# Performance work log

Hardware: AMD Instinct MI355X
Metric: run time of the kernel (lower is better)

The kernel has to match this reference:

```python
import jax, jax.numpy as jnp
import numpy as np

# ---- static config (mirrors CE defaults) ----
PS = 7        # patch size
WS = 27       # search window (per side)
S0 = 4        # query stride (stride0)
KS = 100      # k_s: top-k kept by search
KA = 100      # k_a: top-k used for aggregation
SCALE = 10.0  # softmax_scale
CI = 16       # inter_channels


def conv2d(x, w, b, pad):
    y = jax.lax.conv_general_dilated(
        x, w, (1, 1), [(pad, pad), (pad, pad)],
        dimension_numbers=("NCHW", "OIHW", "NCHW"))
    return y + b[None, :, None, None]


def all_patches(v):
    """[T,C,H,W] -> [T, H*W, C*PS*PS]; top-left anchored PSxPS patches,
    edge-clamped at the border (dnls-style bounded patch extraction)."""
    t, c, h, w = v.shape
    ii = jnp.clip(jnp.arange(h)[:, None] + jnp.arange(PS)[None, :], 0, h - 1)
    jj = jnp.clip(jnp.arange(w)[:, None] + jnp.arange(PS)[None, :], 0, w - 1)
    p = v[:, :, ii][:, :, :, :, jj]          # [T,C,H,PS,W,PS]
    p = p.transpose(0, 2, 4, 1, 3, 5)        # [T,H,W,C,PS,PS]
    return p.reshape(t, h * w, c * PS * PS)


def setup_inputs():
    key = jax.random.key(0)
    ks = jax.random.split(key, 4)
    vid = jax.random.normal(ks[0], (4, 64, 128, 128), jnp.float32)
    g_w = jax.random.normal(ks[1], (CI, 64, 3, 3), jnp.float32) * 0.05
    g_b = jnp.zeros((CI,), jnp.float32)
    theta_w = jax.random.normal(ks[2], (CI, 64, 1, 1), jnp.float32) * 0.1
    theta_b = jnp.zeros((CI,), jnp.float32)
    return {"vid": vid, "g_w": g_w, "g_b": g_b,
            "theta_w": theta_w, "theta_b": theta_b}


def reference(vid, g_w, g_b, theta_w, theta_b):
    t, c, h, w = vid.shape
    nH, nW = h // S0, w // S0
    Q, N = nH * nW, h * w

    # feature extraction (g -> search features, theta -> aggregation values)
    v1 = conv2d(vid, g_w, g_b, 1)          # [T,CI,H,W]
    v2 = conv2d(vid, theta_w, theta_b, 0)  # [T,CI,H,W]

    # windowed k-NN patch search: query grid (stride0) vs all keys (stride1=1)
    P1 = all_patches(v1)                                    # [T,N,D]
    qis = jnp.arange(nH) * S0
    qjs = jnp.arange(nW) * S0
    qflat = (qis[:, None] * w + qjs[None, :]).reshape(-1)   # [Q]
    Pq = P1[:, qflat]                                       # [T,Q,D]
    scores = jnp.einsum("tqd,tnd->tqn", Pq, P1)             # [T,Q,N]

    off = jnp.arange(WS) - WS // 2
    ci = jnp.clip(qis[:, None] + off, 0, h - 1)             # [nH,WS]
    cj = jnp.clip(qjs[:, None] + off, 0, w - 1)             # [nW,WS]
    cand = (ci[:, None, :, None] * w + cj[None, :, None, :]).reshape(Q, WS * WS)
    dists = jnp.take_along_axis(scores, cand[None], axis=2)  # [T,Q,WS*WS]

    d_k, widx = jax.lax.top_k(dists, KS)                    # [T,Q,KS]
    inds = jnp.take_along_axis(jnp.broadcast_to(cand[None], dists.shape),
                               widx, axis=2)                # flat key positions

    # top-k softmax aggregation weights
    wgt = jax.nn.softmax(d_k[..., :KA] * SCALE, axis=-1)    # [T,Q,KA]
    inds_a = inds[..., :KA]

    # wpsum: weighted sum of value patches gathered at neighbor indices,
    # expressed as sparse-scatter matrix @ dense patch matrix
    A = jnp.zeros((t, Q, N), scores.dtype).at[
        jnp.arange(t)[:, None, None],
        jnp.arange(Q)[None, :, None],
        inds_a].add(wgt)                                    # [T,Q,N]
    P2 = all_patches(v2)                                    # [T,N,D]
    z = jnp.einsum("tqn,tnd->tqd", A, P2)                   # [T,Q,CI*PS*PS]

    # ifold: scatter-add overlapping patches + count normalization
    z = z.reshape(t, Q, CI, PS, PS).transpose(0, 2, 1, 3, 4)
    z = z.reshape(t, CI, Q * PS * PS)
    ri = jnp.clip(qis[:, None] + jnp.arange(PS), 0, h - 1)  # [nH,PS]
    rj = jnp.clip(qjs[:, None] + jnp.arange(PS), 0, w - 1)  # [nW,PS]
    pix = (ri[:, None, :, None] * w + rj[None, :, None, :]).reshape(-1)
    Y = jnp.zeros((t, CI, N), z.dtype).at[:, :, pix].add(z)
    Zc = jnp.zeros((N,), z.dtype).at[pix].add(1.0)
    y = (Y / Zc).reshape(t, CI, h, w)
    return y
```

## Files before the change

### kernel.cpp

```cpp
#include <hip/hip_runtime.h>
#include <hip/hip_bf16.h>

#define T_ 4
#define C_ 64
#define H_ 128
#define W_ 128
#define CI_ 16
#define PS_ 7
#define NC_ 729
#define S0_ 4
#define KS_ 100
#define NQ_ 1024
#define SCALE_ 10.0f
#define HW_ (H_*W_)
#define RW_ 45
#define LCAP_ 768
#define CB_ 8

typedef float v2f __attribute__((ext_vector_type(2)));
#if __has_builtin(__builtin_elementwise_fma)
#define VFMA(a, b, c) __builtin_elementwise_fma((a), (b), (c))
#else
#define VFMA(a, b, c) ((a) * (b) + (c))
#endif

__device__ __forceinline__ float4 colfix(float4 r, bool loB, bool hiB) {
  float4 o;
  o.x = loB ? 0.f : (hiB ? r.y : r.x);
  o.y = loB ? r.x : (hiB ? r.z : r.y);
  o.z = loB ? r.y : (hiB ? r.w : r.z);
  o.w = loB ? r.z : (hiB ? 0.f : r.w);
  return o;
}

__global__ __launch_bounds__(128, 1) void conv3x3_kernel(
    const float* __restrict__ vid, const float* __restrict__ gw,
    const float* __restrict__ gb, float4* __restrict__ v1cs) {
  __shared__ float wls[C_ * 9 * 4];
  const int tid = threadIdx.x;
  const int g = blockIdx.y, t = blockIdx.z;
  for (int m = tid; m < C_ * 9 * 4; m += 128) {
    int co = m & 3, ck = m >> 2;
    wls[m] = gw[((size_t)(g * 4 + co) * C_) * 9 + ck];
  }
  __syncthreads();
  const int ti0 = (blockIdx.x >> 3) * 16, tj0 = (blockIdx.x & 7) * 16;
  const int u = tid >> 3, v = tid & 7;
  const int i = ti0 + u, j0 = tj0 + 2 * v;
  const int c0 = j0 - 1;
  const int c0c = min(max(c0, 0), W_ - 4);
  const bool loB = (c0 < 0), hiB = (c0 > W_ - 4);
  const int rm1 = max(i - 1, 0), rp1 = min(i + 1, H_ - 1);
  const float mk0 = (i > 0) ? 1.f : 0.f;
  const float mk2 = (i < H_ - 1) ? 1.f : 0.f;
  const int o0 = rm1 * W_ + c0c, o1 = i * W_ + c0c, o2 = rp1 * W_ + c0c;

  float accA[4], accB[4];
#pragma unroll
  for (int co = 0; co < 4; ++co) { accA[co] = gb[g * 4 + co]; accB[co] = gb[g * 4 + co]; }

  const float* vb = vid + ((size_t)t * C_) * HW_;
#pragma unroll 1
  for (int cb = 0; cb < C_; cb += CB_) {
    float4 r[CB_][3];
#pragma unroll
    for (int c = 0; c < CB_; ++c) {
      const float* p = vb + (size_t)(cb + c) * HW_;
      r[c][0] = *(const float4*)(p + o0);
      r[c][1] = *(const float4*)(p + o1);
      r[c][2] = *(const float4*)(p + o2);
    }
#pragma unroll
    for (int c = 0; c < CB_; ++c) {
      float4 f0 = colfix(r[c][0], loB, hiB);
      float4 f1 = colfix(r[c][1], loB, hiB);
      float4 f2 = colfix(r[c][2], loB, hiB);
      f0.x *= mk0; f0.y *= mk0; f0.z *= mk0; f0.w *= mk0;
      f2.x *= mk2; f2.y *= mk2; f2.z *= mk2; f2.w *= mk2;
      const float* wc = &wls[(cb + c) * 36];
      float e0[4] = {f0.x, f0.y, f0.z, f0.w};
      float e1[4] = {f1.x, f1.y, f1.z, f1.w};
      float e2[4] = {f2.x, f2.y, f2.z, f2.w};
#pragma unroll
      for (int kj = 0; kj < 3; ++kj) {
#pragma unroll
        for (int co = 0; co < 4; ++co) {
          accA[co] = fmaf(wc[(0 * 3 + kj) * 4 + co], e0[kj],     accA[co]);
          accB[co] = fmaf(wc[(0 * 3 + kj) * 4 + co], e0[kj + 1], accB[co]);
          accA[co] = fmaf(wc[(1 * 3 + kj) * 4 + co], e1[kj],     accA[co]);
          accB[co] = fmaf(wc[(1 * 3 + kj) * 4 + co], e1[kj + 1], accB[co]);
          accA[co] = fmaf(wc[(2 * 3 + kj) * 4 + co], e2[kj],     accA[co]);
          accB[co] = fmaf(wc[(2 * 3 + kj) * 4 + co], e2[kj + 1], accB[co]);
        }
      }
    }
  }
  const size_t o = ((size_t)g * T_ + t) * HW_ + i * W_ + j0;
  v1cs[o]     = make_float4(accA[0], accA[1], accA[2], accA[3]);
  v1cs[o + 1] = make_float4(accB[0], accB[1], accB[2], accB[3]);
}

__global__ __launch_bounds__(256, 1) void conv1x1_kernel(
    const float* __restrict__ vid, const float* __restrict__ tw,
    const float* __restrict__ tb, float4* __restrict__ v2cs) {
  __shared__ float w[C_ * 4];
  const int t = blockIdx.y, cc = blockIdx.z;
  for (int m = threadIdx.x; m < C_ * 4; m += 256) {
    int o = m & 3, c = m >> 2;
    w[m] = tw[(cc * 4 + o) * C_ + c];
  }
  __syncthreads();
  const int pix = blockIdx.x * 256 + threadIdx.x;
  float acc[4];
#pragma unroll
  for (int o = 0; o < 4; ++o) acc[o] = tb[cc * 4 + o];
  const float* vb = vid + ((size_t)t * C_) * HW_ + pix;
#pragma unroll 1
  for (int c0 = 0; c0 < C_; c0 += 16) {
    float x[16];
#pragma unroll
    for (int uu = 0; uu < 16; ++uu) x[uu] = vb[(size_t)(c0 + uu) * HW_];
#pragma unroll
    for (int uu = 0; uu < 16; ++uu)
#pragma unroll
      for (int o = 0; o < 4; ++o)
        acc[o] = fmaf(w[(c0 + uu) * 4 + o], x[uu], acc[o]);
  }
  v2cs[((size_t)cc * T_ + t) * HW_ + pix] = make_float4(acc[0], acc[1], acc[2], acc[3]);
}

__global__ __launch_bounds__(512, 2) void dist_kernel(
    const float4* __restrict__ v1cs, float* __restrict__ distG) {
  __shared__ float4 Rs[2][2048];
  const int tid = threadIdx.x;
  const int t = blockIdx.y;
  const int qi0 = (blockIdx.x >> 3) * 16, qj0 = (blockIdx.x & 7) * 16;
  const int w = tid >> 6, lane = tid & 63;
  const int pr = w >> 2, dj = (w & 3) * 4;
  const int rbase = 8 * pr;
  const int qi_p = qi0 + rbase;
  const int qj = qj0 + dj;
  const int la = lane >> 1, bg = lane & 1;
  const int b_lo = max(13 - qj, 0);
  const int bs = bg ? 13 : b_lo;
  const int a_lo0 = max(13 - qi_p, 0);
  const int a_lo1 = max(9 - qi_p, 0);
  const bool compute_ok = (la < 31);

  int soff[4];
#pragma unroll
  for (int k = 0; k < 4; ++k) {
    int p = min(tid + 512 * k, RW_ * RW_ - 1);
    int uu = p / RW_, vv = p - uu * RW_;
    int row = min(max(qi0 - 13 + uu, 0), H_ - 1);
    int col = min(max(qj0 - 13 + vv, 0), W_ - 1);
    soff[k] = row * W_ + col;
  }

  v2f acc0[14], acc1[14];
#pragma unroll
  for (int j = 0; j < 14; ++j) { acc0[j] = (v2f){0.f, 0.f}; acc1[j] = (v2f){0.f, 0.f}; }

  float4 st[4];
  {
    const float4* src = v1cs + ((size_t)0 * T_ + t) * HW_;
#pragma unroll
    for (int k = 0; k < 4; ++k) st[k] = src[soff[k]];
  }
  int cur = 0;
#pragma unroll 1
  for (int cc = 0; cc < 4; ++cc) {
    float4* buf = &Rs[cur][0];
#pragma unroll
    for (int k = 0; k < 4; ++k) buf[tid + 512 * k] = st[k];
    if (cc < 3) {
      const float4* src = v1cs + ((size_t)(cc + 1) * T_ + t) * HW_;
#pragma unroll
      for (int k = 0; k < 4; ++k) st[k] = src[soff[k]];
    }
    __syncthreads();
    if (compute_ok) {
#pragma unroll 1
      for (int r = 0; r < 7; ++r) {
        v2f q0lo[7], q0hi[7], q1lo[7], q1hi[7];
        const float4* q0row = &buf[(rbase + 13 + r) * RW_ + dj + 13];
#pragma unroll
        for (int s = 0; s < 7; ++s) {
          float4 qq = q0row[s];
          q0lo[s] = (v2f){qq.x, qq.y};
          q0hi[s] = (v2f){qq.z, qq.w};
          float4 q2 = q0row[4 * RW_ + s];
          q1lo[s] = (v2f){q2.x, q2.y};
          q1hi[s] = (v2f){q2.z, q2.w};
        }
        const float4* crow = &buf[(rbase + la + r) * RW_ + dj + bs];
#pragma unroll
        for (int y = 0; y < 20; ++y) {
          float4 vv4 = crow[y];
          v2f vlo = (v2f){vv4.x, vv4.y}, vhi = (v2f){vv4.z, vv4.w};
          const int s_lo = (y > 13) ? (y - 13) : 0;
          const int s_hi = (y < 6) ? y : 6;
#pragma unroll
          for (int s = s_lo; s <= s_hi; ++s) {
            int j = y - s;
            acc0[j] = VFMA(q0lo[s], vlo, acc0[j]);
            acc0[j] = VFMA(q0hi[s], vhi, acc0[j]);
            acc1[j] = VFMA(q1lo[s], vlo, acc1[j]);
            acc1[j] = VFMA(q1hi[s], vhi, acc1[j]);
          }
        }
      }
    }
    cur ^= 1;
  }
  if (compute_ok) {
    const int q0q = ((qi_p >> 2) << 5) + (qj >> 2);
    if (la >= a_lo0 && la <= 26) {
      float* out = distG + ((size_t)t * NQ_ + q0q) * NC_ + la * 27 + bs;
#pragma unroll
      for (int j = 0; j < 14; ++j) out[j] = acc0[j].x + acc0[j].y;
    }
    const int a1 = la - 4;
    if (a1 >= a_lo1 && a1 <= 26) {
      float* out = distG + ((size_t)t * NQ_ + (q0q + 32)) * NC_ + a1 * 27 + bs;
#pragma unroll
      for (int j = 0; j < 14; ++j) out[j] = acc1[j].x + acc1[j].y;
    }
  }
}

__global__ __launch_bounds__(256) void select_kernel(
    const float* __restrict__ distG, int* __restrict__ sel_n,
    float* __restrict__ sel_w, float* __restrict__ wsum_out) {
  __shared__ float dist[NC_];
  __shared__ unsigned int ukey[NC_];
  __shared__ float redf[4];
  __shared__ unsigned int hist[256];
  __shared__ int lk[LCAP_];
  __shared__ unsigned int lkey[LCAP_];
  __shared__ unsigned int scal[6];

  const int tid = threadIdx.x;
  const int lane = tid & 63, wid = tid >> 6;
  const int q = blockIdx.x, t = blockIdx.y;
  const int qi = (q >> 5) * S0_, qj = (q & 31) * S0_;
  const int a_lo = max(13 - qi, 0), b_lo = max(13 - qj, 0);
  const size_t base = ((size_t)t * NQ_ + q) * NC_;

  for (int h = tid; h < 256; h += 256) hist[h] = 0;
  if (tid == 0) { scal[2] = 0; scal[3] = 0; }
  float lmax = -INFINITY;
  for (int k = tid; k < NC_; k += 256) {
    int aa = k / 27, bb = k - aa * 27;
    int kk = max(aa, a_lo) * 27 + max(bb, b_lo);
    float d = distG[base + kk];
    dist[k] = d;
    unsigned int u = __float_as_uint(d);
    ukey[k] = u ^ (((unsigned int)((int)u >> 31)) | 0x80000000u);
    lmax = fmaxf(lmax, d);
  }
#pragma unroll
  for (int off = 32; off > 0; off >>= 1)
    lmax = fmaxf(lmax, __shfl_down(lmax, off, 64));
  if (lane == 0) redf[wid] = lmax;
  __syncthreads();
  const float dmax = fmaxf(fmaxf(redf[0], redf[1]), fmaxf(redf[2], redf[3]));
  for (int k = tid; k < NC_; k += 256) atomicAdd(&hist[ukey[k] >> 24], 1u);
  __syncthreads();
  if (wid == 0) {
    int s4 = (int)(hist[lane * 4] + hist[lane * 4 + 1] + hist[lane * 4 + 2] + hist[lane * 4 + 3]);
    int s = s4;
#pragma unroll
    for (int off = 1; off < 64; off <<= 1) {
      int o = __shfl_down(s, off, 64);
      if (lane + off < 64) s += o;
    }
    int above = s - s4;
    if (above < KS_ && s >= KS_) {
      int run = above;
#pragma unroll
      for (int bb = 3; bb >= 0; --bb) {
        int h = (int)hist[lane * 4 + bb];
        if (run + h >= KS_) { scal[0] = (unsigned int)(lane * 4 + bb); scal[1] = (unsigned int)run; break; }
        run += h;
      }
    }
  }
  __syncthreads();
  const unsigned int beta = scal[0];
  const int run = (int)scal[1];
  for (int h = tid; h < 256; h += 256) hist[h] = 0;
  __syncthreads();
  for (int k = tid; k < NC_; k += 256)
    if ((ukey[k] >> 24) == beta) atomicAdd(&hist[(ukey[k] >> 16) & 0xFFu], 1u);
  __syncthreads();
  if (wid == 0) {
    int s4 = (int)(hist[lane * 4] + hist[lane * 4 + 1] + hist[lane * 4 + 2] + hist[lane * 4 + 3]);
    int s = s4;
#pragma unroll
    for (int off = 1; off < 64; off <<= 1) {
      int o = __shfl_down(s, off, 64);
      if (lane + off < 64) s += o;
    }
    int above = run + s - s4;
    if (above < KS_ && run + s >= KS_) {
      int r2 = above;
#pragma unroll
      for (int bb = 3; bb >= 0; --bb) {
        int h = (int)hist[lane * 4 + bb];
        if (r2 + h >= KS_) { scal[4] = (unsigned int)(lane * 4 + bb); scal[5] = (unsigned int)r2; break; }
        r2 += h;
      }
    }
  }
  __syncthreads();
  const unsigned int beta2 = scal[4];
  const int run2 = (int)scal[5];
  const size_t outb = ((size_t)t * NQ_ + q) * KS_;
  float lsum = 0.f;
  for (int k = tid; k < NC_; k += 256) {
    unsigned int key = ukey[k];
    unsigned int bin = key >> 24;
    bool sel = false, bdry = false;
    if (bin > beta) sel = true;
    else if (bin == beta) {
      unsigned int b2 = (key >> 16) & 0xFFu;
      if (b2 > beta2) sel = true;
      else if (b2 == beta2) bdry = true;
    }
    if (sel) {
      unsigned int slot = atomicAdd(&scal[2], 1u);
      int aa = k / 27, bb = k - aa * 27;
      int ni = min(max(qi + aa - 13, 0), H_ - 1);
      int nj = min(max(qj + bb - 13, 0), W_ - 1);
      float wv = __expf(SCALE_ * (dist[k] - dmax));
      sel_n[outb + slot] = (ni << 7) | nj;
      sel_w[outb + slot] = wv;
      lsum += wv;
    } else if (bdry) {
      unsigned int pos = atomicAdd(&scal[3], 1u);
      if (pos < LCAP_) { lk[pos] = k; lkey[pos] = key; }
    }
  }
  __syncthreads();
  const int L = min((int)scal[3], LCAP_);
  for (int i = tid; i < L; i += 256) {
    unsigned int key = lkey[i];
    int k = lk[i];
    int cnt = run2;
    for (int m = 0; m < L; ++m)
      cnt += (int)((lkey[m] > key) || (lkey[m] == key && lk[m] < k));
    if (cnt < KS_) {
      unsigned int slot = atomicAdd(&scal[2], 1u);
      int aa = k / 27, bb = k - aa * 27;
      int ni = min(max(qi + aa - 13, 0), H_ - 1);
      int nj = min(max(qj + bb - 13, 0), W_ - 1);
      float wv = __expf(SCALE_ * (dist[k] - dmax));
      sel_n[outb + slot] = (ni << 7) | nj;
      sel_w[outb + slot] = wv;
      lsum += wv;
    }
  }
#pragma unroll
  for (int off = 32; off > 0; off >>= 1) lsum += __shfl_down(lsum, off, 64);
  __syncthreads();
  if (lane == 0) redf[wid] = lsum;
  __syncthreads();
  if (tid == 0) wsum_out[t * NQ_ + q] = (redf[0] + redf[1]) + (redf[2] + redf[3]);
}

__global__ __launch_bounds__(1024) void agg_kernel(
    const float4* __restrict__ v2cs, const int* __restrict__ sel_n,
    const float* __restrict__ sel_w, const float* __restrict__ wsum,
    float* __restrict__ Y) {
  __shared__ float4 Rs[RW_ * RW_];
  __shared__ int s_off[16][KS_];
  __shared__ float s_w[16][KS_];
  const int tid = threadIdx.x;
  const int t = blockIdx.y;
  const int qi0 = (blockIdx.x >> 3) * 16, qj0 = (blockIdx.x & 7) * 16;
  const int w = tid >> 6, lane = tid & 63;
  const int di = (w >> 2) * 4, dj = (w & 3) * 4;
  const int qi = qi0 + di, qj = qj0 + dj;
  const int q = ((qi >> 2) << 5) + (qj >> 2);
  const size_t base = ((size_t)t * NQ_ + q) * KS_;
  const float inv = 1.0f / wsum[t * NQ_ + q];
  for (int k = lane; k < KS_; k += 64) {
    int n = sel_n[base + k];
    int ni = n >> 7, nj = n & 127;
    s_off[w][k] = (ni - qi0 + 13) * RW_ + (nj - qj0 + 13);
    s_w[w][k] = sel_w[base + k] * inv;
  }
  const int r = lane / 7, s = lane - r * 7;
  const int myo = r * RW_ + s;
  const int oi = min(qi + r, H_ - 1), oj = min(qj + s, W_ - 1);
#pragma unroll 1
  for (int cc = 0; cc < 4; ++cc) {
    __syncthreads();
    const float4* src = v2cs + ((size_t)cc * T_ + t) * HW_;
    for (int p = tid; p < RW_ * RW_; p += 1024) {
      int uu = p / RW_, vv = p - uu * RW_;
      int row = min(max(qi0 - 13 + uu, 0), H_ - 1);
      int col = min(max(qj0 - 13 + vv, 0), W_ - 1);
      Rs[p] = src[row * W_ + col];
    }
    __syncthreads();
    if (lane < 49) {
      float4 acc = make_float4(0.f, 0.f, 0.f, 0.f);
#pragma unroll 4
      for (int k = 0; k < KS_; ++k) {
        float wv = s_w[w][k];
        float4 v = Rs[s_off[w][k] + myo];
        acc.x = fmaf(wv, v.x, acc.x);
        acc.y = fmaf(wv, v.y, acc.y);
        acc.z = fmaf(wv, v.z, acc.z);
        acc.w = fmaf(wv, v.w, acc.w);
      }
      float* yb = Y + (((size_t)t * CI_ + cc * 4) * H_ + oi) * W_ + oj;
      atomicAdd(yb, acc.x);
      atomicAdd(yb + HW_, acc.y);
      atomicAdd(yb + 2 * HW_, acc.z);
      atomicAdd(yb + 3 * HW_, acc.w);
    }
  }
}

__device__ __forceinline__ int cov_axis(int x) {
  int c = 0;
#pragma unroll
  for (int r = 0; r < 7; ++r) {
    if (x < H_ - 1) {
      int qb = x - r;
      c += (qb >= 0 && (qb & 3) == 0) ? 1 : 0;
    } else {
      c += (r >= 3) ? 1 : 0;
    }
  }
  return c;
}

__global__ void norm_kernel(float* __restrict__ Y) {
  int idx = blockIdx.x * blockDim.x + threadIdx.x;
  if (idx >= T_ * CI_ * HW_) return;
  int p = idx & (HW_ - 1);
  float z = (float)(cov_axis(p >> 7) * cov_axis(p & 127));
  Y[idx] /= z;
}

extern "C" void kernel_launch(void* const* d_in, const int* in_sizes, int n_in,
                              void* d_out, int out_size, void* d_ws, size_t ws_size,
                              hipStream_t stream) {
  const float* vid     = (const float*)d_in[0];
  const float* g_w     = (const float*)d_in[1];
  const float* g_b     = (const float*)d_in[2];
  const float* theta_w = (const float*)d_in[3];
  const float* theta_b = (const float*)d_in[4];
  float* Y = (float*)d_out;

  float* v1cs  = (float*)d_ws;
  float* v2cs  = v1cs + (size_t)4 * T_ * HW_ * 4;
  float* distG = v2cs + (size_t)4 * T_ * HW_ * 4;
  int*   sel_n = (int*)(distG + (size_t)T_ * NQ_ * NC_);
  float* sel_w = (float*)(sel_n + (size_t)T_ * NQ_ * KS_);
  float* wsumv = sel_w + (size_t)T_ * NQ_ * KS_;

  hipMemsetAsync(Y, 0, (size_t)out_size * sizeof(float), stream);

  conv3x3_kernel<<<dim3(64, 4, T_), 128, 0, stream>>>(vid, g_w, g_b, (float4*)v1cs);
  conv1x1_kernel<<<dim3(HW_ / 256, T_, 4), 256, 0, stream>>>(vid, theta_w, theta_b, (float4*)v2cs);
  dist_kernel<<<dim3(64, T_), 512, 0, stream>>>((const float4*)v1cs, distG);
  select_kernel<<<dim3(NQ_, T_), 256, 0, stream>>>(distG, sel_n, sel_w, wsumv);
  agg_kernel<<<dim3(64, T_), 1024, 0, stream>>>((const float4*)v2cs, sel_n, sel_w, wsumv, Y);
  norm_kernel<<<(T_ * CI_ * HW_ + 255) / 256, 256, 0, stream>>>(Y);
}
```

Measured before the change: 263.9 us.

## Split dist kernel channel reduction across two blocks with partial sums

The distance kernel's reduction over the four channel groups is split into two halves along a new grid z dimension. Each half writes its partial distances to its own buffer, and the select kernel adds the two partials when it loads them. This doubles the number of blocks (from 256 to 512) to improve GPU fill. Launch bounds are also raised to 4 blocks per SM. The cost is an extra distance buffer write and read, plus possible register pressure from the tighter launch bounds. The split only runs when the workspace is large enough.

```diff
diff --git a/kernel.cpp b/kernel.cpp
--- a/kernel.cpp
+++ b/kernel.cpp
@@ -129,11 +129,14 @@
   v2cs[((size_t)cc * T_ + t) * HW_ + pix] = make_float4(acc[0], acc[1], acc[2], acc[3]);
 }
 
-__global__ __launch_bounds__(512, 2) void dist_kernel(
-    const float4* __restrict__ v1cs, float* __restrict__ distG) {
+__global__ __launch_bounds__(512, 4) void dist_kernel(
+    const float4* __restrict__ v1cs, float* __restrict__ distG,
+    float* __restrict__ distB, int nch) {
   __shared__ float4 Rs[2][2048];
   const int tid = threadIdx.x;
   const int t = blockIdx.y;
+  const int half = blockIdx.z;
+  const int cbase = half * 2;
   const int qi0 = (blockIdx.x >> 3) * 16, qj0 = (blockIdx.x & 7) * 16;
   const int w = tid >> 6, lane = tid & 63;
   const int pr = w >> 2, dj = (w & 3) * 4;
@@ -163,18 +166,18 @@
 
   float4 st[4];
   {
-    const float4* src = v1cs + ((size_t)0 * T_ + t) * HW_;
+    const float4* src = v1cs + ((size_t)cbase * T_ + t) * HW_;
 #pragma unroll
     for (int k = 0; k < 4; ++k) st[k] = src[soff[k]];
   }
   int cur = 0;
 #pragma unroll 1
-  for (int cc = 0; cc < 4; ++cc) {
+  for (int ci = 0; ci < nch; ++ci) {
     float4* buf = &Rs[cur][0];
 #pragma unroll
     for (int k = 0; k < 4; ++k) buf[tid + 512 * k] = st[k];
-    if (cc < 3) {
-      const float4* src = v1cs + ((size_t)(cc + 1) * T_ + t) * HW_;
+    if (ci + 1 < nch) {
+      const float4* src = v1cs + ((size_t)(cbase + ci + 1) * T_ + t) * HW_;
 #pragma unroll
       for (int k = 0; k < 4; ++k) st[k] = src[soff[k]];
     }
@@ -214,15 +217,16 @@
     cur ^= 1;
   }
   if (compute_ok) {
+    float* outB = half ? distB : distG;
     const int q0q = ((qi_p >> 2) << 5) + (qj >> 2);
     if (la >= a_lo0 && la <= 26) {
-      float* out = distG + ((size_t)t * NQ_ + q0q) * NC_ + la * 27 + bs;
+      float* out = outB + ((size_t)t * NQ_ + q0q) * NC_ + la * 27 + bs;
 #pragma unroll
       for (int j = 0; j < 14; ++j) out[j] = acc0[j].x + acc0[j].y;
     }
     const int a1 = la - 4;
     if (a1 >= a_lo1 && a1 <= 26) {
-      float* out = distG + ((size_t)t * NQ_ + (q0q + 32)) * NC_ + a1 * 27 + bs;
+      float* out = outB + ((size_t)t * NQ_ + (q0q + 32)) * NC_ + a1 * 27 + bs;
 #pragma unroll
       for (int j = 0; j < 14; ++j) out[j] = acc1[j].x + acc1[j].y;
     }
@@ -230,8 +234,9 @@
 }
 
 __global__ __launch_bounds__(256) void select_kernel(
-    const float* __restrict__ distG, int* __restrict__ sel_n,
-    float* __restrict__ sel_w, float* __restrict__ wsum_out) {
+    const float* __restrict__ distA, const float* __restrict__ distB, int dual,
+    int* __restrict__ sel_n, float* __restrict__ sel_w,
+    float* __restrict__ wsum_out) {
   __shared__ float dist[NC_];
   __shared__ unsigned int ukey[NC_];
   __shared__ float redf[4];
@@ -253,7 +258,8 @@
   for (int k = tid; k < NC_; k += 256) {
     int aa = k / 27, bb = k - aa * 27;
     int kk = max(aa, a_lo) * 27 + max(bb, b_lo);
-    float d = distG[base + kk];
+    float d = distA[base + kk];
+    if (dual) d += distB[base + kk];
     dist[k] = d;
     unsigned int u = __float_as_uint(d);
     ukey[k] = u ^ (((unsigned int)((int)u >> 31)) | 0x80000000u);
@@ -463,13 +469,20 @@
   int*   sel_n = (int*)(distG + (size_t)T_ * NQ_ * NC_);
   float* sel_w = (float*)(sel_n + (size_t)T_ * NQ_ * KS_);
   float* wsumv = sel_w + (size_t)T_ * NQ_ * KS_;
+  float* distB = wsumv + (size_t)T_ * NQ_;
+
+  const size_t need_dual =
+      ((size_t)4 * T_ * HW_ * 4 * 2 + (size_t)T_ * NQ_ * NC_ * 2 +
+       (size_t)T_ * NQ_ * KS_ * 2 + (size_t)T_ * NQ_) * sizeof(float);
+  const int dual = (ws_size >= need_dual) ? 1 : 0;
 
   hipMemsetAsync(Y, 0, (size_t)out_size * sizeof(float), stream);
 
   conv3x3_kernel<<<dim3(64, 4, T_), 128, 0, stream>>>(vid, g_w, g_b, (float4*)v1cs);
   conv1x1_kernel<<<dim3(HW_ / 256, T_, 4), 256, 0, stream>>>(vid, theta_w, theta_b, (float4*)v2cs);
-  dist_kernel<<<dim3(64, T_), 512, 0, stream>>>((const float4*)v1cs, distG);
-  select_kernel<<<dim3(NQ_, T_), 256, 0, stream>>>(distG, sel_n, sel_w, wsumv);
+  dist_kernel<<<dim3(64, T_, dual ? 2 : 1), 512, 0, stream>>>(
+      (const float4*)v1cs, distG, distB, dual ? 2 : 4);
+  select_kernel<<<dim3(NQ_, T_), 256, 0, stream>>>(distG, distB, dual, sel_n, sel_w, wsumv);
   agg_kernel<<<dim3(64, T_), 1024, 0, stream>>>((const float4*)v2cs, sel_n, sel_w, wsumv, Y);
   norm_kernel<<<(T_ * CI_ * HW_ + 255) / 256, 256, 0, stream>>>(Y);
 }
```

New measurement: 339.4 us. +28.6%, slower.
